# Kernel optimization log

Measured on AMD Instinct MI355X. Metric: run time of the kernel, lower is better.

Reference implementation:

```python
import jax, jax.numpy as jnp
import numpy as np

X_MIN, X_MAX = -3.0, 3.0
EPS = 1e-08


def setup_inputs() -> dict:
    key = jax.random.key(0)
    k1, k2, k3 = jax.random.split(key, 3)
    B, D_in, D_out, K = 8192, 512, 128, 16
    x = jax.random.normal(k1, (B, D_in), dtype=jnp.float32)
    # trunc_normal_(std=0.02) approximated by scaled normal
    weights = jax.random.normal(k2, (D_out, D_in, K), dtype=jnp.float32) * 0.02
    # xavier_uniform for skip
    limit = float(np.sqrt(6.0 / (D_in + D_out)))
    skip_w = jax.random.uniform(k3, (D_out, D_in), dtype=jnp.float32,
                                minval=-limit, maxval=limit)
    bias = jnp.zeros((D_out,), dtype=jnp.float32)
    return {"x": x, "weights": weights, "skip_w": skip_w, "bias": bias}


def reference(x, weights, skip_w, bias):
    # x: (B, D_in); weights: (D_out, D_in, K); skip_w: (D_out, D_in); bias: (D_out,)
    K = weights.shape[-1]
    t = jnp.clip((x - X_MIN) / (X_MAX - X_MIN + EPS), 0.0, 1.0)
    pos = t * (K - 1)
    idx0 = jnp.floor(pos).astype(jnp.int32)
    idx1 = jnp.minimum(idx0 + 1, K - 1)
    frac = jnp.clip(pos - idx0.astype(pos.dtype), 0.0, 1.0)
    # Hat-basis coefficients per (b, i): avoids materializing (B, D_out, D_in)
    oh0 = jax.nn.one_hot(idx0, K, dtype=x.dtype)  # (B, D_in, K)
    oh1 = jax.nn.one_hot(idx1, K, dtype=x.dtype)
    c = oh0 * (1.0 - frac)[..., None] + oh1 * frac[..., None]  # (B, D_in, K)
    # y[b,o] = sum_i (1-frac)*w[o,i,idx0] + frac*w[o,i,idx1]
    y = jnp.einsum('bik,oik->bo', c, weights)
    y = y + bias + x @ skip_w.T
    return y
```

## Files before the change

kernel.cpp:

```cpp
#include <hip/hip_runtime.h>

typedef __attribute__((ext_vector_type(8))) short short8;
typedef __attribute__((ext_vector_type(4))) float f32x4;

#define DIN 512
#define DOUT 128
#define KK 16
#define BTOT 8192
#define KAUG (DIN * KK + DIN)
#define BK 128
#define NCHUNK_TOT (KAUG / BK)
#define NSPL 8
#define BM 64
#define CHUNK_BYTES 32768
#define CBASE 32768
#define LDS_BYTES 49152
#define PART_OFF (4u << 20)
#define OUT_ELEMS (BTOT * DOUT)

__device__ static inline unsigned short f2bf(float x) {
  unsigned u = __builtin_bit_cast(unsigned, x);
  return (unsigned short)((u + 0x7FFFu + ((u >> 16) & 1u)) >> 16);
}

__device__ static inline void llds16(const char* g, char* l) {
  __builtin_amdgcn_global_load_lds(
      (const __attribute__((address_space(1))) unsigned int*)g,
      (__attribute__((address_space(3))) unsigned int*)l, 16, 0, 0);
}

__global__ __launch_bounds__(256) void build_wpp(const float* __restrict__ w,
                                                 const float* __restrict__ sk,
                                                 unsigned short* __restrict__ wpp) {
  const int gi = blockIdx.x * 256 + threadIdx.x;
  const int g = gi >> 11;
  const int rem = gi & 2047;
  const int o = rem >> 4;
  const int kcs = rem & 15;
  const int kc = kcs ^ (o & 15);
  const int kglob = g * 128 + kc * 8;
  const float* src = (kglob < 8192) ? (w + (size_t)o * 8192 + kglob)
                                    : (sk + (size_t)o * 512 + (kglob - 8192));
  const float4 v0 = ((const float4*)src)[0];
  const float4 v1 = ((const float4*)src)[1];
  uint4 pk;
  pk.x = f2bf(v0.x) | ((unsigned)f2bf(v0.y) << 16);
  pk.y = f2bf(v0.z) | ((unsigned)f2bf(v0.w) << 16);
  pk.z = f2bf(v1.x) | ((unsigned)f2bf(v1.y) << 16);
  pk.w = f2bf(v1.z) | ((unsigned)f2bf(v1.w) << 16);
  ((uint4*)wpp)[gi] = pk;
}

__global__ __launch_bounds__(256, 3) void kan_mfma(const float* __restrict__ x,
                                                   const unsigned short* __restrict__ wpp,
                                                   float* __restrict__ part) {
  __shared__ __align__(16) char smem[LDS_BYTES];
  const int tid = threadIdx.x;
  const int bt = blockIdx.x >> 3;
  const int sp = blockIdx.x & 7;
  const int b0 = bt * BM;
  const int wid = tid >> 6, lane = tid & 63;
  const int lr = lane & 15, lq = lane >> 4;
  const int wm = wid & 1, wn = wid >> 1;
  const int g0 = sp * 8 + (sp < 4 ? sp : 4);
  const int gend = g0 + (sp < 4 ? 9 : 8);

  f32x4 acc[2][4] = {};

  auto stageW = [&](int g) {
    const char* gsrc = ((const char*)wpp) + (size_t)g * CHUNK_BYTES + wid * 8192 + lane * 16;
    char* ldst = smem + wid * 8192;
#pragma unroll
    for (int it = 0; it < 8; ++it) llds16(gsrc + it * 1024, ldst + it * 1024);
  };

  auto loadX = [&](int g, float& a, float& b) {
    const int r0 = tid >> 3, il = tid & 7;
    a = x[(size_t)(b0 + r0) * DIN + g * 8 + il];
    b = x[(size_t)(b0 + 32 + r0) * DIN + g * 8 + il];
  };

  auto buildSpline = [&](float xv0, float xv1) {
#pragma unroll
    for (int hh = 0; hh < 2; ++hh) {
      const int bl = (tid >> 3) + hh * 32;
      const int il = tid & 7;
      const float xv = hh ? xv1 : xv0;
      float t = fminf(fmaxf((xv + 3.0f) * (1.0f / 6.0f), 0.0f), 1.0f);
      const float pos = t * 15.0f;
      int i0 = (int)pos;
      i0 = i0 > 14 ? 14 : i0;
      const float f = pos - (float)i0;
      char* row = smem + CBASE + bl * 256;
      const int swz = bl & 15;
      char* gA = row + (((il * 2) ^ swz) << 4);
      char* gB = row + (((il * 2 + 1) ^ swz) << 4);
      *(uint4*)gA = make_uint4(0, 0, 0, 0);
      *(uint4*)gB = make_uint4(0, 0, 0, 0);
      const unsigned short h0 = f2bf(1.0f - f);
      const unsigned short h1 = f2bf(f);
      const int i1 = i0 + 1;
      *(unsigned short*)(((i0 & 8) ? gB : gA) + (i0 & 7) * 2) = h0;
      *(unsigned short*)(((i1 & 8) ? gB : gA) + (i1 & 7) * 2) = h1;
    }
  };

  auto buildSkip = [&](int g) {
    const int ioff = (g - 64) * BK;
    const int bl = tid >> 2, q = tid & 3;
    const float* xr = x + (size_t)(b0 + bl) * DIN + ioff;
    char* row = smem + CBASE + bl * 256;
    const int swz = bl & 15;
#pragma unroll
    for (int gg = 0; gg < 4; ++gg) {
      const int kc = q * 4 + gg;
      const float4 v0 = ((const float4*)(xr + kc * 8))[0];
      const float4 v1 = ((const float4*)(xr + kc * 8))[1];
      uint4 pk;
      pk.x = f2bf(v0.x) | ((unsigned)f2bf(v0.y) << 16);
      pk.y = f2bf(v0.z) | ((unsigned)f2bf(v0.w) << 16);
      pk.z = f2bf(v1.x) | ((unsigned)f2bf(v1.y) << 16);
      pk.w = f2bf(v1.z) | ((unsigned)f2bf(v1.w) << 16);
      *(uint4*)(row + ((kc ^ swz) << 4)) = pk;
    }
  };

  float xa, xb;
  loadX(g0, xa, xb);

  for (int g = g0; g < gend; ++g) {
    __syncthreads();
    stageW(g);
    float na = 0.0f, nb = 0.0f;
    const bool pf = (g + 1 < gend) && (g + 1 < 64);
    if (pf) loadX(g + 1, na, nb);
    if (g < 64) buildSpline(xa, xb);
    else buildSkip(g);
    __syncthreads();
#pragma unroll
    for (int ks = 0; ks < 4; ++ks) {
      const int swq = ((ks * 4 + lq) ^ lr) << 4;
      short8 af[2], bfr[4];
#pragma unroll
      for (int mt = 0; mt < 2; ++mt) {
        const int m = wm * 32 + mt * 16 + lr;
        af[mt] = *(const short8*)(smem + CBASE + m * 256 + swq);
      }
#pragma unroll
      for (int nt = 0; nt < 4; ++nt) {
        const int o = wn * 64 + nt * 16 + lr;
        bfr[nt] = *(const short8*)(smem + o * 256 + swq);
      }
#pragma unroll
      for (int mt = 0; mt < 2; ++mt)
#pragma unroll
        for (int nt = 0; nt < 4; ++nt)
          acc[mt][nt] = __builtin_amdgcn_mfma_f32_16x16x32_bf16(af[mt], bfr[nt], acc[mt][nt], 0, 0, 0);
    }
    if (pf) { xa = na; xb = nb; }
  }

  float* p = part + (size_t)sp * OUT_ELEMS;
#pragma unroll
  for (int nt = 0; nt < 4; ++nt) {
    const int col = wn * 64 + nt * 16 + lr;
#pragma unroll
    for (int mt = 0; mt < 2; ++mt) {
      const int rowb = b0 + wm * 32 + mt * 16 + lq * 4;
#pragma unroll
      for (int r = 0; r < 4; ++r)
        p[(size_t)(rowb + r) * DOUT + col] = acc[mt][nt][r];
    }
  }
}

__global__ __launch_bounds__(256) void kan_reduce(const float4* __restrict__ part,
                                                  const float* __restrict__ bias,
                                                  float4* __restrict__ out) {
  const int id = blockIdx.x * 256 + threadIdx.x;
  float4 s = part[id];
#pragma unroll
  for (int sp = 1; sp < NSPL; ++sp) {
    const float4 v = part[(size_t)sp * (OUT_ELEMS / 4) + id];
    s.x += v.x; s.y += v.y; s.z += v.z; s.w += v.w;
  }
  const float4 bv = ((const float4*)bias)[id & 31];
  s.x += bv.x; s.y += bv.y; s.z += bv.z; s.w += bv.w;
  out[id] = s;
}

__global__ void kan_naive(const float* __restrict__ x, const float* __restrict__ w,
                          const float* __restrict__ skw, const float* __restrict__ bias,
                          float* __restrict__ out) {
  const int b = blockIdx.x;
  const int o = threadIdx.x;
  float acc = bias[o];
  for (int i = 0; i < DIN; ++i) {
    float xv = x[(size_t)b * DIN + i];
    float t = fminf(fmaxf((xv + 3.0f) * (1.0f / 6.0f), 0.0f), 1.0f);
    float p = t * 15.0f;
    float fi = floorf(p);
    int i0 = (int)fi;
    int i1 = (i0 < 15) ? i0 + 1 : 15;
    float f = p - fi;
    const float* wr = &w[((size_t)o * DIN + i) * KK];
    acc += (1.0f - f) * wr[i0] + f * wr[i1] + xv * skw[(size_t)o * DIN + i];
  }
  out[(size_t)b * DOUT + o] = acc;
}

extern "C" void kernel_launch(void* const* d_in, const int* in_sizes, int n_in,
                              void* d_out, int out_size, void* d_ws, size_t ws_size,
                              hipStream_t stream) {
  const float* x    = (const float*)d_in[0];
  const float* w    = (const float*)d_in[1];
  const float* skw  = (const float*)d_in[2];
  const float* bias = (const float*)d_in[3];
  float* out = (float*)d_out;

  const size_t need = PART_OFF + (size_t)NSPL * OUT_ELEMS * sizeof(float);
  if (ws_size < need) {
    kan_naive<<<BTOT, DOUT, 0, stream>>>(x, w, skw, bias, out);
    return;
  }

  unsigned short* wpp = (unsigned short*)d_ws;
  float* part = (float*)((char*)d_ws + PART_OFF);

  build_wpp<<<NCHUNK_TOT * 2048 / 256, 256, 0, stream>>>(w, skw, wpp);
  kan_mfma<<<(BTOT / BM) * NSPL, 256, 0, stream>>>(x, wpp, part);
  kan_reduce<<<OUT_ELEMS / 4 / 256, 256, 0, stream>>>((const float4*)part, bias,
                                                      (float4*)out);
}
```

Before: 113.1 us.

## Double M-tile to 128 rows and replace partial-sum reduce kernel with atomics

Doubles the batch tile per block from 64 to 128 rows, so each staged weight chunk feeds twice as many MFMAs. This halves global weight traffic per output, at the cost of more LDS and lower occupancy (launch bound 2). The split-K partial buffer and separate reduce kernel are removed. Each split instead atomically adds into a zeroed output, with split 0 adding the bias and a rotated column order to spread atomic contention. This adds a memset, float atomic traffic, and nondeterministic summation order.

```diff
diff --git a/kernel.cpp b/kernel.cpp
--- a/kernel.cpp
+++ b/kernel.cpp
@@ -11,12 +11,10 @@
 #define BK 128
 #define NCHUNK_TOT (KAUG / BK)
 #define NSPL 8
-#define BM 64
+#define BM 128
 #define CHUNK_BYTES 32768
 #define CBASE 32768
-#define LDS_BYTES 49152
-#define PART_OFF (4u << 20)
-#define OUT_ELEMS (BTOT * DOUT)
+#define LDS_BYTES 65536
 
 __device__ static inline unsigned short f2bf(float x) {
   unsigned u = __builtin_bit_cast(unsigned, x);
@@ -51,21 +49,22 @@
   ((uint4*)wpp)[gi] = pk;
 }
 
-__global__ __launch_bounds__(256, 3) void kan_mfma(const float* __restrict__ x,
+__global__ __launch_bounds__(256, 2) void kan_mfma(const float* __restrict__ x,
                                                    const unsigned short* __restrict__ wpp,
-                                                   float* __restrict__ part) {
+                                                   const float* __restrict__ bias,
+                                                   float* __restrict__ out) {
   __shared__ __align__(16) char smem[LDS_BYTES];
   const int tid = threadIdx.x;
-  const int bt = blockIdx.x >> 3;
-  const int sp = blockIdx.x & 7;
+  const int sp = blockIdx.x >> 6;
+  const int bt = blockIdx.x & 63;
   const int b0 = bt * BM;
   const int wid = tid >> 6, lane = tid & 63;
   const int lr = lane & 15, lq = lane >> 4;
-  const int wm = wid & 1, wn = wid >> 1;
+  const int wm = wid >> 1, wn = wid & 1;
   const int g0 = sp * 8 + (sp < 4 ? sp : 4);
   const int gend = g0 + (sp < 4 ? 9 : 8);
 
-  f32x4 acc[2][4] = {};
+  f32x4 acc[4][4] = {};
 
   auto stageW = [&](int g) {
     const char* gsrc = ((const char*)wpp) + (size_t)g * CHUNK_BYTES + wid * 8192 + lane * 16;
@@ -74,18 +73,19 @@
     for (int it = 0; it < 8; ++it) llds16(gsrc + it * 1024, ldst + it * 1024);
   };
 
-  auto loadX = [&](int g, float& a, float& b) {
+  auto loadX = [&](int g, float (&v)[4]) {
     const int r0 = tid >> 3, il = tid & 7;
-    a = x[(size_t)(b0 + r0) * DIN + g * 8 + il];
-    b = x[(size_t)(b0 + 32 + r0) * DIN + g * 8 + il];
-  };
-
-  auto buildSpline = [&](float xv0, float xv1) {
-#pragma unroll
-    for (int hh = 0; hh < 2; ++hh) {
+#pragma unroll
+    for (int hh = 0; hh < 4; ++hh)
+      v[hh] = x[(size_t)(b0 + r0 + hh * 32) * DIN + g * 8 + il];
+  };
+
+  auto buildSpline = [&](const float (&v)[4]) {
+#pragma unroll
+    for (int hh = 0; hh < 4; ++hh) {
       const int bl = (tid >> 3) + hh * 32;
       const int il = tid & 7;
-      const float xv = hh ? xv1 : xv0;
+      const float xv = v[hh];
       float t = fminf(fmaxf((xv + 3.0f) * (1.0f / 6.0f), 0.0f), 1.0f);
       const float pos = t * 15.0f;
       int i0 = (int)pos;
@@ -107,13 +107,13 @@
 
   auto buildSkip = [&](int g) {
     const int ioff = (g - 64) * BK;
-    const int bl = tid >> 2, q = tid & 3;
+    const int bl = tid >> 1, q = tid & 1;
     const float* xr = x + (size_t)(b0 + bl) * DIN + ioff;
     char* row = smem + CBASE + bl * 256;
     const int swz = bl & 15;
 #pragma unroll
-    for (int gg = 0; gg < 4; ++gg) {
-      const int kc = q * 4 + gg;
+    for (int gg = 0; gg < 8; ++gg) {
+      const int kc = q * 8 + gg;
       const float4 v0 = ((const float4*)(xr + kc * 8))[0];
       const float4 v1 = ((const float4*)(xr + kc * 8))[1];
       uint4 pk;
@@ -125,25 +125,26 @@
     }
   };
 
-  float xa, xb;
-  loadX(g0, xa, xb);
+  float xa[4];
+  loadX(g0, xa);
 
   for (int g = g0; g < gend; ++g) {
     __syncthreads();
     stageW(g);
-    float na = 0.0f, nb = 0.0f;
+    float xn[4] = {};
     const bool pf = (g + 1 < gend) && (g + 1 < 64);
-    if (pf) loadX(g + 1, na, nb);
-    if (g < 64) buildSpline(xa, xb);
+    if (pf) loadX(g + 1, xn);
+    if (g < 64) buildSpline(xa);
     else buildSkip(g);
     __syncthreads();
+
 #pragma unroll
     for (int ks = 0; ks < 4; ++ks) {
       const int swq = ((ks * 4 + lq) ^ lr) << 4;
-      short8 af[2], bfr[4];
-#pragma unroll
-      for (int mt = 0; mt < 2; ++mt) {
-        const int m = wm * 32 + mt * 16 + lr;
+      short8 af[4], bfr[4];
+#pragma unroll
+      for (int mt = 0; mt < 4; ++mt) {
+        const int m = wm * 64 + mt * 16 + lr;
         af[mt] = *(const short8*)(smem + CBASE + m * 256 + swq);
       }
 #pragma unroll
@@ -152,41 +153,30 @@
         bfr[nt] = *(const short8*)(smem + o * 256 + swq);
       }
 #pragma unroll
-      for (int mt = 0; mt < 2; ++mt)
+      for (int mt = 0; mt < 4; ++mt)
 #pragma unroll
         for (int nt = 0; nt < 4; ++nt)
           acc[mt][nt] = __builtin_amdgcn_mfma_f32_16x16x32_bf16(af[mt], bfr[nt], acc[mt][nt], 0, 0, 0);
     }
-    if (pf) { xa = na; xb = nb; }
-  }
-
-  float* p = part + (size_t)sp * OUT_ELEMS;
-#pragma unroll
-  for (int nt = 0; nt < 4; ++nt) {
+    if (pf) {
+#pragma unroll
+      for (int hh = 0; hh < 4; ++hh) xa[hh] = xn[hh];
+    }
+  }
+
+#pragma unroll
+  for (int ntl = 0; ntl < 4; ++ntl) {
+    const int nt = (ntl + sp) & 3;
     const int col = wn * 64 + nt * 16 + lr;
-#pragma unroll
-    for (int mt = 0; mt < 2; ++mt) {
-      const int rowb = b0 + wm * 32 + mt * 16 + lq * 4;
+    const float bv = (sp == 0) ? bias[col] : 0.0f;
+#pragma unroll
+    for (int mt = 0; mt < 4; ++mt) {
+      const int rowb = b0 + wm * 64 + mt * 16 + lq * 4;
 #pragma unroll
       for (int r = 0; r < 4; ++r)
-        p[(size_t)(rowb + r) * DOUT + col] = acc[mt][nt][r];
-    }
-  }
-}
-
-__global__ __launch_bounds__(256) void kan_reduce(const float4* __restrict__ part,
-                                                  const float* __restrict__ bias,
-                                                  float4* __restrict__ out) {
-  const int id = blockIdx.x * 256 + threadIdx.x;
-  float4 s = part[id];
-#pragma unroll
-  for (int sp = 1; sp < NSPL; ++sp) {
-    const float4 v = part[(size_t)sp * (OUT_ELEMS / 4) + id];
-    s.x += v.x; s.y += v.y; s.z += v.z; s.w += v.w;
-  }
-  const float4 bv = ((const float4*)bias)[id & 31];
-  s.x += bv.x; s.y += bv.y; s.z += bv.z; s.w += bv.w;
-  out[id] = s;
+        atomicAdd(out + (size_t)(rowb + r) * DOUT + col, acc[mt][nt][r] + bv);
+    }
+  }
 }
 
 __global__ void kan_naive(const float* __restrict__ x, const float* __restrict__ w,
@@ -218,17 +208,15 @@
   const float* bias = (const float*)d_in[3];
   float* out = (float*)d_out;
 
-  const size_t need = PART_OFF + (size_t)NSPL * OUT_ELEMS * sizeof(float);
+  const size_t need = (size_t)NCHUNK_TOT * CHUNK_BYTES;
   if (ws_size < need) {
     kan_naive<<<BTOT, DOUT, 0, stream>>>(x, w, skw, bias, out);
     return;
   }
 
   unsigned short* wpp = (unsigned short*)d_ws;
-  float* part = (float*)((char*)d_ws + PART_OFF);
-
+
+  hipMemsetAsync(d_out, 0, (size_t)out_size * sizeof(float), stream);
   build_wpp<<<NCHUNK_TOT * 2048 / 256, 256, 0, stream>>>(w, skw, wpp);
-  kan_mfma<<<(BTOT / BM) * NSPL, 256, 0, stream>>>(x, wpp, part);
-  kan_reduce<<<OUT_ELEMS / 4 / 256, 256, 0, stream>>>((const float4*)part, bias,
-                                                      (float4*)out);
-}
+  kan_mfma<<<NSPL * (BTOT / BM), 256, 0, stream>>>(x, wpp, bias, out);
+}
```

Result: slower. 263.4 us (+132.9%).
